# Performance work log

Measured on AMD Instinct MI355X. Metric: run time of the kernel, lower is better.

The kernel has to match this reference:

```python
import jax, jax.numpy as jnp
import numpy as np

D_MODEL = 64
D_INNER = 128
D_STATE = 16
D_CONV = 4
DT_RANK = 4
P_PIX = 5
HH = 120
WW = 120


def _layernorm(x, g, b):
    m = x.mean(-1, keepdims=True)
    v = ((x - m) ** 2).mean(-1, keepdims=True)
    return (x - m) * jax.lax.rsqrt(v + 1e-5) * g + b


def _ssm_scan(delta, Bm, Cm, u, A):
    # delta,u: (b,L,d); Bm,Cm: (b,L,n); A: (d,n)
    def step(h, inp):
        dt, bt, ct, ut = inp  # (b,d),(b,n),(b,n),(b,d)
        h = h * jnp.exp(dt[:, :, None] * A) + (dt * ut)[:, :, None] * bt[:, None, :]
        return h, jnp.einsum('bdn,bn->bd', h, ct)
    h0 = jnp.zeros((u.shape[0], A.shape[0], A.shape[1]), u.dtype)
    xs = (jnp.swapaxes(delta, 0, 1), jnp.swapaxes(Bm, 0, 1),
          jnp.swapaxes(Cm, 0, 1), jnp.swapaxes(u, 0, 1))
    _, ys = jax.lax.scan(step, h0, xs)
    return jnp.swapaxes(ys, 0, 1)  # (b,L,d)


def _mamba(p, x):
    # faithful mamba_ssm Mamba with use_fast_path=False, out_proj=Identity
    in_w, conv_w, conv_b, xproj_w, dt_w, dt_b, A_log, Dv = p
    L = x.shape[1]
    xz = jnp.einsum('bld,ed->ble', x, in_w)  # (b,L,2*d_inner)
    xh, z = xz[..., :D_INNER], xz[..., D_INNER:]
    xp = jnp.pad(xh, ((0, 0), (D_CONV - 1, 0), (0, 0)))  # causal depthwise conv
    conv = conv_b + sum(xp[:, i:i + L, :] * conv_w[:, i] for i in range(D_CONV))
    xh = jax.nn.silu(conv)
    dbl = jnp.einsum('bld,ed->ble', xh, xproj_w)
    dt = dbl[..., :DT_RANK]
    Bm = dbl[..., DT_RANK:DT_RANK + D_STATE]
    Cm = dbl[..., DT_RANK + D_STATE:]
    delta = jax.nn.softplus(jnp.einsum('blr,dr->bld', dt, dt_w) + dt_b)
    A = -jnp.exp(A_log)
    y = _ssm_scan(delta, Bm, Cm, xh, A) + xh * Dv
    return y * jax.nn.silu(z)


def _bidir(p2, xn):
    inp = jnp.stack([xn, xn[:, ::-1]])  # forward + flipped sequence
    ys = jax.vmap(_mamba, in_axes=(0, 0))(p2, inp)
    return ys[0], ys[1]


def _pixel(x, p2, g, b, out_w):
    B, C, Hh, Ww = x.shape
    p = P_PIX
    NH, NW = Hh // p, Ww // p
    L = NH * NW
    xd = x.reshape(B, C, NH, p, NW, p).transpose(0, 3, 5, 1, 2, 4).reshape(B * p * p, C, L)
    xn = _layernorm(jnp.swapaxes(xd, 1, 2), g, b)
    yf, yb = _bidir(p2, xn)
    yo = jnp.einsum('bld,cd->blc', yf + yb[:, ::-1], out_w)
    xo = jnp.swapaxes(yo, 1, 2).reshape(B, p, p, C, NH, NW).transpose(0, 3, 4, 1, 5, 2).reshape(B, C, Hh, Ww)
    return xo + x


def _window(x, p2, g, b, out_w, out_bw):
    # window p==1: AvgPool(1)/Upsample(1) are identities
    B, C, Hh, Ww = x.shape
    L = Hh * Ww
    xn = _layernorm(jnp.swapaxes(x.reshape(B, C, L), 1, 2), g, b)
    yf, yb = _bidir(p2, xn)
    xM = jnp.einsum('bld,cd->bcl', yf, out_w)
    yM = jnp.einsum('bld,cd->bcl', yb, out_bw)
    xo = jnp.einsum('bld,cd->blc', yf + yb[:, ::-1], out_w)
    return jnp.swapaxes(xo, 1, 2).reshape(B, C, Hh, Ww) + x, xM, yM


def _edges(M, step=32):
    hub = np.arange(0, M, step)
    ii, jj = np.meshgrid(hub, hub, indexing='ij')
    mask = ii != jj
    # off-diagonal hub-hub edges + self loops for every node (GCNConv add_remaining_self_loops)
    src = np.concatenate([ii[mask], np.arange(M)])
    dst = np.concatenate([jj[mask], np.arange(M)])
    deg = np.bincount(dst, minlength=M).astype(np.float32)
    norm = (deg[src] ** -0.5) * (deg[dst] ** -0.5)
    return jnp.asarray(src), jnp.asarray(dst), jnp.asarray(norm, jnp.float32)


def _gcn(x, Wm, bv, src, dst, norm, M):
    h = jnp.einsum('bmf,gf->bmg', x, Wm)
    msg = h[:, src, :] * norm[None, :, None]          # (B,E,g)
    agg = jax.ops.segment_sum(jnp.swapaxes(msg, 0, 1), dst, num_segments=M)
    return jnp.swapaxes(agg, 0, 1) + bv


def setup_inputs() -> dict:
    key = jax.random.key(0)
    ks = iter(jax.random.split(key, 48))
    def rn(shape, scale=1.0):
        return jax.random.normal(next(ks), shape, jnp.float32) * scale
    d = {}
    d['x'] = rn((1, D_MODEL, HH, WW))
    for pre in ('pix', 'win'):
        d[pre + '_in_w'] = rn((4, 2, 2 * D_INNER, D_MODEL), D_MODEL ** -0.5)
        d[pre + '_conv_w'] = rn((4, 2, D_INNER, D_CONV), 0.3)
        d[pre + '_conv_b'] = rn((4, 2, D_INNER), 0.02)
        d[pre + '_xproj_w'] = rn((4, 2, DT_RANK + 2 * D_STATE, D_INNER), D_INNER ** -0.5)
        d[pre + '_dt_w'] = rn((4, 2, D_INNER, DT_RANK), DT_RANK ** -0.5)
        d[pre + '_dt_b'] = jax.random.uniform(next(ks), (4, 2, D_INNER), jnp.float32, -5.0, -3.0)
        d[pre + '_A_log'] = jnp.log(jax.random.uniform(next(ks), (4, 2, D_INNER, D_STATE), jnp.float32, 1.0, 16.0))
        d[pre + '_D'] = rn((4, 2, D_INNER), 0.5)
        d[pre + '_ln_g'] = jnp.ones((4, D_MODEL), jnp.float32)
        d[pre + '_ln_b'] = jnp.zeros((4, D_MODEL), jnp.float32)
    d['pix_out_w'] = rn((4, D_MODEL, D_INNER), D_INNER ** -0.5)
    d['win_out_w'] = rn((4, D_MODEL, D_INNER), D_INNER ** -0.5)
    d['win_out_bw'] = rn((4, D_MODEL, D_INNER), D_INNER ** -0.5)
    d['gcn_w1'] = rn((2 * D_MODEL, 4 * D_MODEL), (4 * D_MODEL) ** -0.5)
    d['gcn_b1'] = jnp.zeros((2 * D_MODEL,), jnp.float32)
    d['gcn_w2'] = rn((D_MODEL, 2 * D_MODEL), (2 * D_MODEL) ** -0.5)
    d['gcn_b2'] = jnp.zeros((D_MODEL,), jnp.float32)
    return d


def reference(x, pix_in_w, pix_conv_w, pix_conv_b, pix_xproj_w, pix_dt_w, pix_dt_b, pix_A_log, pix_D,
              win_in_w, win_conv_w, win_conv_b, win_xproj_w, win_dt_w, win_dt_b, win_A_log, win_D,
              pix_ln_g, pix_ln_b, win_ln_g, win_ln_b, pix_out_w, win_out_w, win_out_bw,
              gcn_w1, gcn_b1, gcn_w2, gcn_b2):
    pix_stack = (pix_in_w, pix_conv_w, pix_conv_b, pix_xproj_w, pix_dt_w, pix_dt_b, pix_A_log, pix_D)
    win_stack = (win_in_w, win_conv_w, win_conv_b, win_xproj_w, win_dt_w, win_dt_b, win_A_log, win_D)
    def pick(stack, i):
        return tuple(t[i] for t in stack)
    def branch(x0, base):
        lastx, xM, yM = x0, None, None
        for s in range(2):
            i = base + s
            a = _pixel(lastx, pick(pix_stack, i), pix_ln_g[i], pix_ln_b[i], pix_out_w[i])
            a, xM, yM = _window(a, pick(win_stack, i), win_ln_g[i], win_ln_b[i], win_out_w[i], win_out_bw[i])
            lastx = lastx + a
        return lastx, xM, yM
    old = x
    lastx, xM, yM = branch(x, 0)
    lastx_T, xMT, yMT = branch(jnp.swapaxes(x, 2, 3), 2)
    B, C, Hh, Ww = x.shape
    M = Hh * Ww
    nf = jnp.swapaxes(jnp.concatenate([xM, yM, xMT, yMT], axis=1), 1, 2)  # (B,M,4C)
    src, dst, norm = _edges(M)
    h = jax.nn.relu(_gcn(nf, gcn_w1, gcn_b1, src, dst, norm, M))
    g = _gcn(h, gcn_w2, gcn_b2, src, dst, norm, M)
    gcn_x = jnp.swapaxes(g, 1, 2).reshape(B, C, Hh, Ww)
    return gcn_x + old + lastx + jnp.swapaxes(lastx_T, 2, 3)
```

## Files before the change

kernel.cpp:

```cpp
#include <hip/hip_runtime.h>
#include <hip/hip_bf16.h>

#define MT 14400
#define WNC 300
#define WCL 48
#define PT 16

typedef unsigned short u16;

__device__ __forceinline__ float b2f(u16 u){
  union { unsigned int i; float f; } v; v.i = ((unsigned int)u) << 16; return v.f;
}
__device__ __forceinline__ u16 f2b(float f){
  union { unsigned int i; float f; } v; v.f = f;
  unsigned int x = v.i;
  return (u16)((x + 0x7fffu + ((x >> 16) & 1u)) >> 16);
}
__device__ __forceinline__ unsigned int pk2(float a, float b){
  return (unsigned int)f2b(a) | ((unsigned int)f2b(b) << 16);
}
__device__ __forceinline__ void st8(float* p, uint4 v){
  *(float4*)p = make_float4(b2f((u16)v.x), b2f((u16)(v.x >> 16)), b2f((u16)v.y), b2f((u16)(v.y >> 16)));
  *(float4*)(p + 4) = make_float4(b2f((u16)v.z), b2f((u16)(v.z >> 16)), b2f((u16)v.w), b2f((u16)(v.w >> 16)));
}
__device__ __forceinline__ float siluf(float x){ return x / (1.f + expf(-x)); }
__device__ __forceinline__ float softplusf(float x){ return (x > 20.f) ? x : log1pf(expf(x)); }

__global__ __launch_bounds__(256) void k_detect(const u16* __restrict__ a, int n, int* __restrict__ flag){
  __shared__ int found;
  if (threadIdx.x == 0) found = 0;
  __syncthreads();
  int f = 0;
  for (int i = threadIdx.x; i < n; i += 256){
    float v = b2f(a[i]);
    if (!(fabsf(v) <= 1e9f)) f = 1;
  }
  if (f) atomicOr(&found, 1);
  __syncthreads();
  if (threadIdx.x == 0) *flag = found;
}

struct PTab {
  const void* src[27];
  float* dst[27];
  int n[27];
  int neg[27];
};

__global__ __launch_bounds__(256) void k_cvt(PTab tb, const int* __restrict__ flag){
  int id = blockIdx.y;
  int n = tb.n[id];
  int fp32 = *flag;
  float* d = tb.dst[id];
  int ng = tb.neg[id];
  for (int i = blockIdx.x * 256 + threadIdx.x; i < n; i += gridDim.x * 256){
    float v = fp32 ? ((const float*)tb.src[id])[i] : b2f(((const u16*)tb.src[id])[i]);
    if (ng) v = -expf(v) * 1.4426950408889634f;
    d[i] = v;
  }
}

__global__ __launch_bounds__(256) void k_wtrans(const float* __restrict__ Wpix, const float* __restrict__ Wwin,
                                                float* __restrict__ WTpix, float* __restrict__ WTwin){
  int mat = blockIdx.y;
  const float* src = (mat < 8) ? (Wpix + (size_t)mat * 16384) : (Wwin + (size_t)(mat - 8) * 16384);
  float* dst = (mat < 8) ? (WTpix + (size_t)mat * 16384) : (WTwin + (size_t)(mat - 8) * 16384);
  int idx = blockIdx.x * 256 + threadIdx.x;
  int e = idx >> 6, k = idx & 63;
  dst[k * 256 + e] = src[idx];
}

__global__ __launch_bounds__(256) void k_gcn1w(const float* __restrict__ ow, const float* __restrict__ obw,
                                               const float* __restrict__ G1, float* __restrict__ W1c){
  int str = blockIdx.y;
  int g = str >> 1, d = str & 1;
  int i2 = g * 2 + 1;
  const float* W = (d ? obw : ow) + (size_t)(i2 * 64) * 128;
  int idx = blockIdx.x * 256 + threadIdx.x;
  int kk = idx >> 7, f = idx & 127;
  float acc = 0.f;
  #pragma unroll 8
  for (int c = 0; c < 64; c++)
    acc += W[(size_t)c * 128 + kk] * G1[(size_t)f * 256 + str * 64 + c];
  W1c[((size_t)str * 128 + kk) * 128 + f] = acc;
}

__global__ __launch_bounds__(256) void k_cvt_x(const void* __restrict__ x, float* __restrict__ imgA,
                                               const int* __restrict__ flag){
  int idx = blockIdx.x * 256 + threadIdx.x;
  int l = idx % MT, c = idx / MT;
  float v = (*flag) ? ((const float*)x)[idx] : b2f(((const u16*)x)[idx]);
  imgA[idx] = v;
  imgA[(size_t)64 * MT + (size_t)c * MT + (l % 120) * 120 + l / 120] = v;
}

__global__ __launch_bounds__(256) void k_inproj(const float* __restrict__ img, const float* __restrict__ lng,
                                                const float* __restrict__ lnb, const float* __restrict__ WT,
                                                u16* __restrict__ xh, u16* __restrict__ z,
                                                int s, int pixelMode){
  int gd = blockIdx.y, g = gd >> 1, dir = gd & 1;
  int i2 = (g * 2 + s) * 2 + dir;
  int iln = g * 2 + s;
  int ttile = blockIdx.x >> 1, ntile = blockIdx.x & 1;
  int t0 = ttile * 64;
  const float* WTm = WT + (size_t)i2 * 16384 + ntile * 128;

  __shared__ __align__(16) float sAT[64 * 68];
  __shared__ __align__(16) float sB[64 * 128];
  __shared__ float ps[4][64], pq[4][64];
  int tid = threadIdx.x;
  int w = tid >> 6, lane = tid & 63;

  {
    int tq = t0 + lane, src = tq;
    if (dir){
      if (pixelMode){ int b = tq / 576, l = tq % 576; src = b * 576 + 575 - l; }
      else src = MT - 1 - tq;
    }
    int hw;
    if (pixelMode){
      int b = src / 576, l = src % 576;
      int ph = b / 5, pw = b % 5, nh = l / 24, nw = l % 24;
      hw = (nh * 5 + ph) * 120 + (nw * 5 + pw);
    } else hw = src;
    const float* base = img + (size_t)g * 64 * MT + hw;
    float sum = 0.f, sq = 0.f;
    #pragma unroll
    for (int j = 0; j < 16; j++){
      int c = w * 16 + j;
      float v = base[(size_t)c * MT];
      sAT[c * 68 + lane] = v;
      sum += v; sq += v * v;
    }
    ps[w][lane] = sum; pq[w][lane] = sq;
  }
  {
    #pragma unroll
    for (int it = 0; it < 8; it++){
      int idx = it * 256 + tid;
      int k = idx >> 5, e4 = (idx & 31) * 4;
      float4 v = *(const float4*)&WTm[(size_t)k * 256 + e4];
      *(float4*)&sB[k * 128 + e4] = v;
    }
  }
  __syncthreads();
  {
    float tot = ps[0][lane] + ps[1][lane] + ps[2][lane] + ps[3][lane];
    float tq2 = pq[0][lane] + pq[1][lane] + pq[2][lane] + pq[3][lane];
    float mean = tot * (1.f / 64.f);
    float var = tq2 * (1.f / 64.f) - mean * mean;
    float rs = rsqrtf(fmaxf(var, 0.f) + 1e-5f);
    #pragma unroll
    for (int j = 0; j < 16; j++){
      int c = w * 16 + j;
      float v = sAT[c * 68 + lane];
      sAT[c * 68 + lane] = (v - mean) * rs * lng[iln * 64 + c] + lnb[iln * 64 + c];
    }
  }
  __syncthreads();

  int tr = tid >> 4, tc = tid & 15;
  float acc[4][8];
  #pragma unroll
  for (int i = 0; i < 4; i++)
    #pragma unroll
    for (int j = 0; j < 8; j++) acc[i][j] = 0.f;

  for (int k0 = 0; k0 < 64; k0 += 4){
    #pragma unroll
    for (int kk = 0; kk < 4; kk++){
      float4 at = *(const float4*)&sAT[(k0 + kk) * 68 + tr * 4];
      float4 b0 = *(const float4*)&sB[(k0 + kk) * 128 + tc * 8];
      float4 b1 = *(const float4*)&sB[(k0 + kk) * 128 + tc * 8 + 4];
      float bv[8] = {b0.x, b0.y, b0.z, b0.w, b1.x, b1.y, b1.z, b1.w};
      #pragma unroll
      for (int i = 0; i < 4; i++){
        float av = ((const float*)&at)[i];
        #pragma unroll
        for (int j = 0; j < 8; j++) acc[i][j] += av * bv[j];
      }
    }
  }

  u16* dst = ntile ? z : xh;
  #pragma unroll
  for (int i = 0; i < 4; i++){
    int t_out = t0 + tr * 4 + i;
    size_t base = (size_t)gd * MT * 128 + (size_t)t_out * 128 + tc * 8;
    uint4 o;
    o.x = pk2(acc[i][0], acc[i][1]); o.y = pk2(acc[i][2], acc[i][3]);
    o.z = pk2(acc[i][4], acc[i][5]); o.w = pk2(acc[i][6], acc[i][7]);
    *(uint4*)&dst[base] = o;
  }
}

__global__ __launch_bounds__(256) void k_xproj(const u16* __restrict__ raw, const float* __restrict__ cw,
                                               const float* __restrict__ cb, const float* __restrict__ xpb,
                                               const float* __restrict__ dtw, const float* __restrict__ dtb,
                                               u16* __restrict__ delta, u16* __restrict__ Bm,
                                               u16* __restrict__ Cm, u16* __restrict__ xhs,
                                               int s, int pixelMode){
  int gd = blockIdx.y, g = gd >> 1, dir = gd & 1;
  int i2 = (g * 2 + s) * 2 + dir;
  const float* XP = xpb + (size_t)i2 * 36 * 128;
  const float* DW = dtw + (size_t)i2 * 128 * 4;
  const float* DB = dtb + (size_t)i2 * 128;
  int t0 = blockIdx.x * 64;
  int SL = pixelMode ? 576 : MT;
  int posBase = t0 % SL;
  size_t gb = (size_t)gd * MT * 128;
  size_t gb16 = (size_t)gd * MT * 16;
  const u16* rawg = raw + gb;

  __shared__ __align__(16) float sX[64 * 132];
  __shared__ __align__(16) float sW[36 * 132];
  float* sDbl = sX;
  int tid = threadIdx.x;

  #pragma unroll
  for (int it = 0; it < 8; it++){
    int idx = it * 256 + tid;
    int tok = idx >> 5, k4 = (idx & 31) * 4;
    int t = t0 + tok, pos = posBase + tok;
    const float4* wr0 = (const float4*)&cw[(size_t)(i2 * 128 + k4) * 4];
    float4 w0 = wr0[0], w1 = wr0[1], w2 = wr0[2], w3 = wr0[3];
    float4 cbv = *(const float4*)&cb[i2 * 128 + k4];
    float a0 = cbv.x, a1 = cbv.y, a2 = cbv.z, a3 = cbv.w;
    #pragma unroll
    for (int i = 0; i < 4; i++){
      int d = 3 - i;
      if (pos >= d){
        uint2 rv = *(const uint2*)&rawg[(size_t)(t - d) * 128 + k4];
        float r0 = b2f((u16)rv.x), r1 = b2f((u16)(rv.x >> 16));
        float r2 = b2f((u16)rv.y), r3 = b2f((u16)(rv.y >> 16));
        a0 += r0 * ((const float*)&w0)[i];
        a1 += r1 * ((const float*)&w1)[i];
        a2 += r2 * ((const float*)&w2)[i];
        a3 += r3 * ((const float*)&w3)[i];
      }
    }
    a0 = siluf(a0); a1 = siluf(a1); a2 = siluf(a2); a3 = siluf(a3);
    *(float4*)&sX[tok * 132 + k4] = make_float4(a0, a1, a2, a3);
    uint2 o; o.x = pk2(a0, a1); o.y = pk2(a2, a3);
    *(uint2*)&xhs[gb + (size_t)t * 128 + k4] = o;
  }
  for (int idx = tid; idx < 36 * 32; idx += 256){
    int out = idx >> 5, k4 = (idx & 31) * 4;
    *(float4*)&sW[out * 132 + k4] = *(const float4*)&XP[(size_t)out * 128 + k4];
  }
  __syncthreads();

  int tr = tid >> 4, tc = tid & 15;
  float acc[4][3];
  #pragma unroll
  for (int i = 0; i < 4; i++){ acc[i][0]=0.f; acc[i][1]=0.f; acc[i][2]=0.f; }
  int o0 = tc * 3;     if (o0 > 35) o0 = 35;
  int o1 = tc * 3 + 1; if (o1 > 35) o1 = 35;
  int o2 = tc * 3 + 2; if (o2 > 35) o2 = 35;

  for (int k0 = 0; k0 < 128; k0 += 4){
    float4 a4[4], bw[3];
    #pragma unroll
    for (int i = 0; i < 4; i++) a4[i] = *(const float4*)&sX[(tr * 4 + i) * 132 + k0];
    bw[0] = *(const float4*)&sW[o0 * 132 + k0];
    bw[1] = *(const float4*)&sW[o1 * 132 + k0];
    bw[2] = *(const float4*)&sW[o2 * 132 + k0];
    #pragma unroll
    for (int kk = 0; kk < 4; kk++){
      #pragma unroll
      for (int i = 0; i < 4; i++){
        float av = ((const float*)&a4[i])[kk];
        #pragma unroll
        for (int j = 0; j < 3; j++) acc[i][j] += av * ((const float*)&bw[j])[kk];
      }
    }
  }
  __syncthreads();

  #pragma unroll
  for (int i = 0; i < 4; i++){
    #pragma unroll
    for (int j = 0; j < 3; j++){
      int out = tc * 3 + j;
      if (out < 36) sDbl[(tr * 4 + i) * 52 + out] = acc[i][j];
    }
  }
  __syncthreads();

  {
    int d = tid & 127, half = tid >> 7;
    float4 dw = *(const float4*)&DW[(size_t)d * 4];
    float db = DB[d];
    #pragma unroll
    for (int it = 0; it < 32; it++){
      int t = it * 2 + half;
      const float* row = &sDbl[t * 52];
      float v = db + row[0] * dw.x + row[1] * dw.y + row[2] * dw.z + row[3] * dw.w;
      delta[gb + (size_t)(t0 + t) * 128 + d] = f2b(softplusf(v));
    }
  }
  #pragma unroll
  for (int it = 0; it < 8; it++){
    int flat = it * 256 + tid;
    int t = flat >> 5, n = flat & 31;
    float v = sDbl[t * 52 + 4 + n];
    if (n < 16) Bm[gb16 + (size_t)(t0 + t) * 16 + n] = f2b(v);
    else        Cm[gb16 + (size_t)(t0 + t) * 16 + (n - 16)] = f2b(v);
  }
}

__global__ __launch_bounds__(256) void k_scan_p1(const u16* __restrict__ delta, const u16* __restrict__ xhs,
                                                 const u16* __restrict__ Bm, const float* __restrict__ A2b,
                                                 float* __restrict__ Acar, float* __restrict__ Bcar, int s){
  int gd = blockIdx.y, g = gd >> 1, dir = gd & 1;
  int i2 = (g * 2 + s) * 2 + dir;
  int chunk = blockIdx.x;
  int tid = threadIdx.x, ch = tid >> 1, nb = (tid & 1) * 8;
  float A2[8], ap[8], bc[8];
  #pragma unroll
  for (int j = 0; j < 8; j++){
    A2[j] = A2b[((size_t)i2 * 128 + ch) * 16 + nb + j];
    ap[j] = 1.f; bc[j] = 0.f;
  }
  size_t so = (size_t)gd * MT * 128 + (size_t)chunk * WCL * 128;
  size_t bo = (size_t)gd * MT * 16  + (size_t)chunk * WCL * 16;
  __shared__ __align__(16) float sd[PT * 128];
  __shared__ __align__(16) float su[PT * 128];
  __shared__ __align__(16) float sb[PT * 16];
  uint4 rd, ru; float rbf;
  rd = *(const uint4*)&delta[so + 8 * (size_t)tid];
  ru = *(const uint4*)&xhs[so + 8 * (size_t)tid];
  rbf = b2f(Bm[bo + tid]);
  const int NT = WCL / PT;
  for (int tile = 0; tile < NT; tile++){
    __syncthreads();
    st8(&sd[8 * tid], rd);
    st8(&su[8 * tid], ru);
    sb[tid] = rbf;
    __syncthreads();
    if (tile + 1 < NT){
      rd = *(const uint4*)&delta[so + (size_t)(tile + 1) * PT * 128 + 8 * (size_t)tid];
      ru = *(const uint4*)&xhs[so + (size_t)(tile + 1) * PT * 128 + 8 * (size_t)tid];
      rbf = b2f(Bm[bo + (size_t)(tile + 1) * PT * 16 + tid]);
    }
    #pragma unroll
    for (int t = 0; t < PT; t++){
      float dt = sd[t * 128 + ch];
      float u  = su[t * 128 + ch];
      float du = dt * u;
      #pragma unroll
      for (int j = 0; j < 8; j++){
        float e = exp2f(dt * A2[j]);
        bc[j] = bc[j] * e + du * sb[t * 16 + nb + j];
        ap[j] *= e;
      }
    }
  }
  size_t o = ((size_t)gd * WNC + chunk) * 2048 + (size_t)ch * 16 + nb;
  float4* A4 = (float4*)(Acar + o);
  float4* B4 = (float4*)(Bcar + o);
  A4[0] = make_float4(ap[0], ap[1], ap[2], ap[3]);
  A4[1] = make_float4(ap[4], ap[5], ap[6], ap[7]);
  B4[0] = make_float4(bc[0], bc[1], bc[2], bc[3]);
  B4[1] = make_float4(bc[4], bc[5], bc[6], bc[7]);
}

__global__ __launch_bounds__(256) void k_scan_p2(const float* __restrict__ Acar, const float* __restrict__ Bcar,
                                                 float* __restrict__ Hin, int resetPeriod){
  int flat = blockIdx.x * 256 + threadIdx.x;
  int cs = flat & 2047, gd = flat >> 11;
  float h = 0.f;
  int cnt = 0;
  for (int c = 0; c < WNC; c++){
    if (cnt == resetPeriod) { h = 0.f; cnt = 0; }
    cnt++;
    size_t o = ((size_t)gd * WNC + c) * 2048 + cs;
    Hin[o] = h;
    h = Acar[o] * h + Bcar[o];
  }
}

__global__ __launch_bounds__(256) void k_scan_p3(const u16* __restrict__ delta, const u16* __restrict__ xhs,
                                                 const u16* __restrict__ Bm, const u16* __restrict__ Cm,
                                                 const u16* __restrict__ zz, const float* __restrict__ A2b,
                                                 const float* __restrict__ Db, const float* __restrict__ Hin,
                                                 u16* __restrict__ ys, int s){
  int gd = blockIdx.y, g = gd >> 1, dir = gd & 1;
  int i2 = (g * 2 + s) * 2 + dir;
  int chunk = blockIdx.x;
  int tid = threadIdx.x, ch = tid >> 1, nb = (tid & 1) * 8;
  float A2[8], h[8];
  size_t ho = ((size_t)gd * WNC + chunk) * 2048 + (size_t)ch * 16 + nb;
  {
    const float4* H4 = (const float4*)(Hin + ho);
    float4 h0 = H4[0], h1 = H4[1];
    h[0]=h0.x; h[1]=h0.y; h[2]=h0.z; h[3]=h0.w;
    h[4]=h1.x; h[5]=h1.y; h[6]=h1.z; h[7]=h1.w;
  }
  #pragma unroll
  for (int j = 0; j < 8; j++) A2[j] = A2b[((size_t)i2 * 128 + ch) * 16 + nb + j];
  float Dv = Db[(size_t)i2 * 128 + ch];
  size_t so = (size_t)gd * MT * 128 + (size_t)chunk * WCL * 128;
  size_t bo = (size_t)gd * MT * 16  + (size_t)chunk * WCL * 16;
  __shared__ __align__(16) float sd[PT * 128];
  __shared__ __align__(16) float su[PT * 128];
  __shared__ __align__(16) float sb[PT * 16];
  __shared__ __align__(16) float sc[PT * 16];
  __shared__ __align__(16) float sy[PT * 128];
  uint4 rd, ru; float rbf, rcf;
  rd = *(const uint4*)&delta[so + 8 * (size_t)tid];
  ru = *(const uint4*)&xhs[so + 8 * (size_t)tid];
  rbf = b2f(Bm[bo + tid]); rcf = b2f(Cm[bo + tid]);
  const int NT = WCL / PT;
  for (int tile = 0; tile < NT; tile++){
    __syncthreads();
    st8(&sd[8 * tid], rd);
    st8(&su[8 * tid], ru);
    sb[tid] = rbf; sc[tid] = rcf;
    __syncthreads();
    if (tile + 1 < NT){
      rd = *(const uint4*)&delta[so + (size_t)(tile + 1) * PT * 128 + 8 * (size_t)tid];
      ru = *(const uint4*)&xhs[so + (size_t)(tile + 1) * PT * 128 + 8 * (size_t)tid];
      rbf = b2f(Bm[bo + (size_t)(tile + 1) * PT * 16 + tid]);
      rcf = b2f(Cm[bo + (size_t)(tile + 1) * PT * 16 + tid]);
    }
    #pragma unroll
    for (int t = 0; t < PT; t++){
      float dt = sd[t * 128 + ch];
      float u  = su[t * 128 + ch];
      float du = dt * u;
      float acc = 0.f;
      #pragma unroll
      for (int j = 0; j < 8; j++){
        float e = exp2f(dt * A2[j]);
        h[j] = h[j] * e + du * sb[t * 16 + nb + j];
        acc += h[j] * sc[t * 16 + nb + j];
      }
      acc += __shfl_xor(acc, 1);
      if (!(tid & 1)) sy[t * 128 + ch] = acc + u * Dv;
    }
    __syncthreads();
    {
      uint4 zv = *(const uint4*)&zz[so + (size_t)tile * PT * 128 + 8 * (size_t)tid];
      const float* py = &sy[8 * tid];
      float y[8];
      y[0] = py[0] * siluf(b2f((u16)zv.x));       y[1] = py[1] * siluf(b2f((u16)(zv.x >> 16)));
      y[2] = py[2] * siluf(b2f((u16)zv.y));       y[3] = py[3] * siluf(b2f((u16)(zv.y >> 16)));
      y[4] = py[4] * siluf(b2f((u16)zv.z));       y[5] = py[5] * siluf(b2f((u16)(zv.z >> 16)));
      y[6] = py[6] * siluf(b2f((u16)zv.w));       y[7] = py[7] * siluf(b2f((u16)(zv.w >> 16)));
      uint4 o;
      o.x = pk2(y[0], y[1]); o.y = pk2(y[2], y[3]); o.z = pk2(y[4], y[5]); o.w = pk2(y[6], y[7]);
      *(uint4*)&ys[so + (size_t)tile * PT * 128 + 8 * (size_t)tid] = o;
    }
    __syncthreads();
  }
}

__global__ __launch_bounds__(256) void k_outproj_pixel(const u16* __restrict__ ys, const float* __restrict__ owb,
                                                       const float* __restrict__ imgA, float* __restrict__ imgB, int s){
  int g = blockIdx.y;
  int i2 = g * 2 + s;
  int tile = blockIdx.x;
  int t0 = tile * 64;
  int b = tile / 9, l0 = (tile % 9) * 64;
  const float* W = owb + (size_t)(i2 * 64) * 128;
  const u16* Yf = ys + (size_t)(g * 2 + 0) * MT * 128;
  const u16* Yb = ys + (size_t)(g * 2 + 1) * MT * 128;
  __shared__ __align__(16) float sA[64 * 36];
  __shared__ __align__(16) float sW[32 * 68];
  __shared__ __align__(16) float sO[64 * 68];
  int tid = threadIdx.x;
  int tr = tid >> 4, tc = tid & 15;
  float acc[4][4];
  #pragma unroll
  for (int i = 0; i < 4; i++){ acc[i][0]=0.f; acc[i][1]=0.f; acc[i][2]=0.f; acc[i][3]=0.f; }

  for (int kt = 0; kt < 4; kt++){
    int k0 = kt * 32;
    {
      int t = tid >> 2, f8 = (tid & 3) * 8;
      int rt = b * 576 + 575 - (l0 + t);
      uint4 vf = *(const uint4*)&Yf[(size_t)(t0 + t) * 128 + k0 + f8];
      uint4 vb = *(const uint4*)&Yb[(size_t)rt * 128 + k0 + f8];
      float* pa = &sA[t * 36 + f8];
      pa[0] = b2f((u16)vf.x) + b2f((u16)vb.x);
      pa[1] = b2f((u16)(vf.x >> 16)) + b2f((u16)(vb.x >> 16));
      pa[2] = b2f((u16)vf.y) + b2f((u16)vb.y);
      pa[3] = b2f((u16)(vf.y >> 16)) + b2f((u16)(vb.y >> 16));
      pa[4] = b2f((u16)vf.z) + b2f((u16)vb.z);
      pa[5] = b2f((u16)(vf.z >> 16)) + b2f((u16)(vb.z >> 16));
      pa[6] = b2f((u16)vf.w) + b2f((u16)vb.w);
      pa[7] = b2f((u16)(vf.w >> 16)) + b2f((u16)(vb.w >> 16));
    }
    {
      int c = tid >> 2, f8 = (tid & 3) * 8;
      const float* wr = &W[(size_t)c * 128 + k0 + f8];
      #pragma unroll
      for (int j = 0; j < 8; j++) sW[(f8 + j) * 68 + c] = wr[j];
    }
    __syncthreads();
    #pragma unroll
    for (int k4 = 0; k4 < 32; k4 += 4){
      float4 a[4];
      #pragma unroll
      for (int i = 0; i < 4; i++) a[i] = *(const float4*)&sA[(tr * 4 + i) * 36 + k4];
      #pragma unroll
      for (int kk = 0; kk < 4; kk++){
        float4 bv = *(const float4*)&sW[(k4 + kk) * 68 + tc * 4];
        #pragma unroll
        for (int i = 0; i < 4; i++){
          float av = ((const float*)&a[i])[kk];
          acc[i][0] += av * bv.x; acc[i][1] += av * bv.y;
          acc[i][2] += av * bv.z; acc[i][3] += av * bv.w;
        }
      }
    }
    __syncthreads();
  }
  #pragma unroll
  for (int j = 0; j < 4; j++)
    *(float4*)&sO[(tc * 4 + j) * 68 + tr * 4] = make_float4(acc[0][j], acc[1][j], acc[2][j], acc[3][j]);
  __syncthreads();
  {
    int c = tid >> 2, q = tid & 3;
    int ph = b / 5, pw = b % 5;
    size_t base = (size_t)g * 64 * MT + (size_t)c * MT;
    #pragma unroll
    for (int v = 0; v < 16; v++){
      int l = l0 + q * 16 + v;
      int nh = l / 24, nw = l % 24;
      size_t io = base + (nh * 5 + ph) * 120 + (nw * 5 + pw);
      imgB[io] = imgA[io] + sO[c * 68 + q * 16 + v];
    }
  }
}

__global__ __launch_bounds__(256) void k_outproj_win(const u16* __restrict__ ys, const float* __restrict__ owb,
                                                     float* __restrict__ imgA, float* __restrict__ imgB, int s){
  int g = blockIdx.y;
  int i2 = g * 2 + s;
  int t0 = blockIdx.x * 64;
  const float* W = owb + (size_t)(i2 * 64) * 128;
  const u16* Yf = ys + (size_t)(g * 2 + 0) * MT * 128;
  const u16* Yb = ys + (size_t)(g * 2 + 1) * MT * 128;
  __shared__ __align__(16) float sA[64 * 36];
  __shared__ __align__(16) float sW[32 * 68];
  __shared__ __align__(16) float sO[64 * 68];
  int tid = threadIdx.x;
  int tr = tid >> 4, tc = tid & 15;
  float acc[4][4];
  #pragma unroll
  for (int i = 0; i < 4; i++){ acc[i][0]=0.f; acc[i][1]=0.f; acc[i][2]=0.f; acc[i][3]=0.f; }

  for (int kt = 0; kt < 4; kt++){
    int k0 = kt * 32;
    {
      int t = tid >> 2, f8 = (tid & 3) * 8;
      int l = t0 + t;
      uint4 vf = *(const uint4*)&Yf[(size_t)l * 128 + k0 + f8];
      uint4 vb = *(const uint4*)&Yb[(size_t)(MT - 1 - l) * 128 + k0 + f8];
      float* pa = &sA[t * 36 + f8];
      pa[0] = b2f((u16)vf.x) + b2f((u16)vb.x);
      pa[1] = b2f((u16)(vf.x >> 16)) + b2f((u16)(vb.x >> 16));
      pa[2] = b2f((u16)vf.y) + b2f((u16)vb.y);
      pa[3] = b2f((u16)(vf.y >> 16)) + b2f((u16)(vb.y >> 16));
      pa[4] = b2f((u16)vf.z) + b2f((u16)vb.z);
      pa[5] = b2f((u16)(vf.z >> 16)) + b2f((u16)(vb.z >> 16));
      pa[6] = b2f((u16)vf.w) + b2f((u16)vb.w);
      pa[7] = b2f((u16)(vf.w >> 16)) + b2f((u16)(vb.w >> 16));
    }
    {
      int c = tid >> 2, f8 = (tid & 3) * 8;
      const float* wr = &W[(size_t)c * 128 + k0 + f8];
      #pragma unroll
      for (int j = 0; j < 8; j++) sW[(f8 + j) * 68 + c] = wr[j];
    }
    __syncthreads();
    #pragma unroll
    for (int k4 = 0; k4 < 32; k4 += 4){
      float4 a[4];
      #pragma unroll
      for (int i = 0; i < 4; i++) a[i] = *(const float4*)&sA[(tr * 4 + i) * 36 + k4];
      #pragma unroll
      for (int kk = 0; kk < 4; kk++){
        float4 bv = *(const float4*)&sW[(k4 + kk) * 68 + tc * 4];
        #pragma unroll
        for (int i = 0; i < 4; i++){
          float av = ((const float*)&a[i])[kk];
          acc[i][0] += av * bv.x; acc[i][1] += av * bv.y;
          acc[i][2] += av * bv.z; acc[i][3] += av * bv.w;
        }
      }
    }
    __syncthreads();
  }
  #pragma unroll
  for (int j = 0; j < 4; j++)
    *(float4*)&sO[(tc * 4 + j) * 68 + tr * 4] = make_float4(acc[0][j], acc[1][j], acc[2][j], acc[3][j]);
  __syncthreads();
  {
    int c = tid >> 2, q = tid & 3;
    size_t base = (size_t)g * 64 * MT + (size_t)c * MT + t0 + q * 16;
    float* pB = &imgB[base];
    float* pA = &imgA[base];
    const float* pS = &sO[c * 68 + q * 16];
    #pragma unroll
    for (int v = 0; v < 4; v++){
      float4 d = *(const float4*)&pS[v * 4];
      float4 bb = *(const float4*)&pB[v * 4];
      bb.x += d.x; bb.y += d.y; bb.z += d.z; bb.w += d.w;
      *(float4*)&pB[v * 4] = bb;
      float4 aa = *(const float4*)&pA[v * 4];
      aa.x += bb.x; aa.y += bb.y; aa.z += bb.z; aa.w += bb.w;
      *(float4*)&pA[v * 4] = aa;
    }
  }
}

__global__ __launch_bounds__(256) void k_gcn1(const u16* __restrict__ ys, const float* __restrict__ W1c,
                                              float* __restrict__ t1){
  int t0 = blockIdx.x * 64;
  __shared__ __align__(16) float sA[64 * 36];
  __shared__ __align__(16) float sB[32 * 132];
  int tid = threadIdx.x, tr = tid >> 4, tc = tid & 15;
  float acc[4][8];
  #pragma unroll
  for (int i = 0; i < 4; i++)
    #pragma unroll
    for (int j = 0; j < 8; j++) acc[i][j] = 0.f;

  for (int kt = 0; kt < 16; kt++){
    int str = kt >> 2, k0 = (kt & 3) * 32;
    const u16* Y = ys + (size_t)str * MT * 128;
    {
      int t = tid >> 2, f8 = (tid & 3) * 8;
      uint4 p = *(const uint4*)&Y[(size_t)(t0 + t) * 128 + k0 + f8];
      st8(&sA[t * 36 + f8], p);
    }
    {
      const float* Wc = W1c + ((size_t)str * 128 + k0) * 128;
      int kk = tid >> 3, f16 = (tid & 7) * 16;
      #pragma unroll
      for (int v = 0; v < 4; v++)
        *(float4*)&sB[kk * 132 + f16 + v * 4] = *(const float4*)&Wc[(size_t)kk * 128 + f16 + v * 4];
    }
    __syncthreads();
    #pragma unroll
    for (int k4 = 0; k4 < 32; k4 += 4){
      float4 a[4];
      #pragma unroll
      for (int i = 0; i < 4; i++) a[i] = *(const float4*)&sA[(tr * 4 + i) * 36 + k4];
      #pragma unroll
      for (int kk = 0; kk < 4; kk++){
        float4 b0 = *(const float4*)&sB[(k4 + kk) * 132 + tc * 8];
        float4 b1 = *(const float4*)&sB[(k4 + kk) * 132 + tc * 8 + 4];
        float bv[8] = {b0.x, b0.y, b0.z, b0.w, b1.x, b1.y, b1.z, b1.w};
        #pragma unroll
        for (int i = 0; i < 4; i++){
          float av = ((const float*)&a[i])[kk];
          #pragma unroll
          for (int j = 0; j < 8; j++) acc[i][j] += av * bv[j];
        }
      }
    }
    __syncthreads();
  }
  #pragma unroll
  for (int i = 0; i < 4; i++){
    size_t base = (size_t)(t0 + tr * 4 + i) * 128 + tc * 8;
    *(float4*)&t1[base]     = make_float4(acc[i][0], acc[i][1], acc[i][2], acc[i][3]);
    *(float4*)&t1[base + 4] = make_float4(acc[i][4], acc[i][5], acc[i][6], acc[i][7]);
  }
}

__global__ __launch_bounds__(128) void k_hub1(const float* __restrict__ t1, float* __restrict__ hubm){
  int f = threadIdx.x;
  float sum = 0.f;
  for (int hb = 0; hb < 450; hb++) sum += t1[(size_t)(hb * 32) * 128 + f];
  hubm[f] = sum * (1.f / 450.f);
}

__global__ __launch_bounds__(256) void k_gcn2(const float* __restrict__ t1, const float* __restrict__ hubm,
                                              const float* __restrict__ b1, const float* __restrict__ W2,
                                              float* __restrict__ t2){
  int t0 = blockIdx.x * 64;
  __shared__ __align__(16) float sA[64 * 36];
  __shared__ __align__(16) float sW[32 * 68];
  int tid = threadIdx.x, tr = tid >> 4, tc = tid & 15;
  float acc[4][4];
  #pragma unroll
  for (int i = 0; i < 4; i++){ acc[i][0]=0.f; acc[i][1]=0.f; acc[i][2]=0.f; acc[i][3]=0.f; }

  for (int kt = 0; kt < 4; kt++){
    int k0 = kt * 32;
    {
      int t = tid >> 2, f8 = (tid & 3) * 8;
      int l = t0 + t;
      const float* src = ((l & 31) == 0) ? &hubm[k0 + f8] : &t1[(size_t)l * 128 + k0 + f8];
      #pragma unroll
      for (int j = 0; j < 8; j++)
        sA[t * 36 + f8 + j] = fmaxf(src[j] + b1[k0 + f8 + j], 0.f);
    }
    {
      int c = tid >> 2, f8 = (tid & 3) * 8;
      const float* wr = &W2[(size_t)c * 128 + k0 + f8];
      #pragma unroll
      for (int j = 0; j < 8; j++) sW[(f8 + j) * 68 + c] = wr[j];
    }
    __syncthreads();
    #pragma unroll
    for (int k4 = 0; k4 < 32; k4 += 4){
      float4 a[4];
      #pragma unroll
      for (int i = 0; i < 4; i++) a[i] = *(const float4*)&sA[(tr * 4 + i) * 36 + k4];
      #pragma unroll
      for (int kk = 0; kk < 4; kk++){
        float4 bv = *(const float4*)&sW[(k4 + kk) * 68 + tc * 4];
        #pragma unroll
        for (int i = 0; i < 4; i++){
          float av = ((const float*)&a[i])[kk];
          acc[i][0] += av * bv.x; acc[i][1] += av * bv.y;
          acc[i][2] += av * bv.z; acc[i][3] += av * bv.w;
        }
      }
    }
    __syncthreads();
  }
  #pragma unroll
  for (int i = 0; i < 4; i++)
    *(float4*)&t2[(size_t)(t0 + tr * 4 + i) * 64 + tc * 4] = make_float4(acc[i][0], acc[i][1], acc[i][2], acc[i][3]);
}

__global__ __launch_bounds__(64) void k_hub2(const float* __restrict__ t2, float* __restrict__ hubm2){
  int c = threadIdx.x;
  float sum = 0.f;
  for (int hb = 0; hb < 450; hb++) sum += t2[(size_t)(hb * 32) * 64 + c];
  hubm2[c] = sum * (1.f / 450.f);
}

__global__ __launch_bounds__(256) void k_final(const void* __restrict__ x, const float* __restrict__ t2,
                                               const float* __restrict__ hubm2, const float* __restrict__ b2,
                                               const float* __restrict__ imgA, void* __restrict__ out,
                                               const int* __restrict__ flag){
  int idx = blockIdx.x * 256 + threadIdx.x;
  int l = idx % MT, c = idx / MT;
  int fp32 = *flag;
  float gval = (((l & 31) == 0) ? hubm2[c] : t2[(size_t)l * 64 + c]) + b2[c];
  float a0 = imgA[idx];
  float a1 = imgA[(size_t)64 * MT + (size_t)c * MT + (l % 120) * 120 + l / 120];
  float xv = fp32 ? ((const float*)x)[idx] : b2f(((const u16*)x)[idx]);
  float val = gval + xv + a0 + a1;
  if (fp32) ((float*)out)[idx] = val;
  else      ((u16*)out)[idx] = f2b(val);
}

extern "C" void kernel_launch(void* const* d_in, const int* in_sizes, int n_in,
                              void* d_out, int out_size, void* d_ws, size_t ws_size,
                              hipStream_t stream){
  int I_X=0,I_PIW=1,I_PCW=2,I_PCB=3,I_PXP=4,I_PDTW=5,I_PDTB=6,I_PAL=7,I_PD=8,I_PLG=9,I_PLB=10,
      I_WIW=11,I_WCW=12,I_WCB=13,I_WXP=14,I_WDTW=15,I_WDTB=16,I_WAL=17,I_WD=18,I_WLG=19,I_WLB=20,
      I_POW=21,I_WOW=22,I_WOBW=23,I_G1=24,I_GB1=25,I_G2=26,I_GB2=27;
  if (n_in >= 28 && in_sizes[9] == 131072){
    I_WIW=9;I_WCW=10;I_WCB=11;I_WXP=12;I_WDTW=13;I_WDTB=14;I_WAL=15;I_WD=16;
    I_PLG=17;I_PLB=18;I_WLG=19;I_WLB=20;
  }
  if (n_in < 28 || in_sizes[I_PIW] != 131072 || out_size != 921600) return;

  float* Wp = (float*)d_ws;
  size_t off = 0;
  auto alloc = [&](size_t n){ size_t r = off; off += (n + 63) & ~(size_t)63; return r; };
  size_t oFlag=alloc(64);
  size_t oPIW=alloc(131072), oPCW=alloc(4096), oPCB=alloc(1024), oPXP=alloc(36864),
         oPDTW=alloc(4096), oPDTB=alloc(1024), oPA=alloc(16384), oPD=alloc(1024),
         oPLG=alloc(256), oPLB=alloc(256);
  size_t oWIW=alloc(131072), oWCW=alloc(4096), oWCB=alloc(1024), oWXP=alloc(36864),
         oWDTW=alloc(4096), oWDTB=alloc(1024), oWA=alloc(16384), oWD=alloc(1024),
         oWLG=alloc(256), oWLB=alloc(256);
  size_t oPOW=alloc(32768), oWOW=alloc(32768), oWOBW=alloc(32768),
         oG1=alloc(32768), oGB1=alloc(128), oG2=alloc(8192), oGB2=alloc(64);
  size_t oPIWT=alloc(131072), oWIWT=alloc(131072), oW1C=alloc(65536);
  size_t oImgA=alloc(2UL*64*MT), oImgB=alloc(2UL*64*MT);
  size_t oRaw=alloc(2UL*MT*128);
  size_t oZ=alloc(2UL*MT*128), oXhs=alloc(2UL*MT*128), oDelta=alloc(2UL*MT*128);
  size_t oBm=alloc(2UL*MT*16), oCm=alloc(2UL*MT*16);
  size_t oAc=alloc(4UL*WNC*2048), oBc=alloc(4UL*WNC*2048), oHin=alloc(4UL*WNC*2048);
  size_t oT1=alloc((size_t)MT*128), oHub1=alloc(128), oT2=alloc((size_t)MT*64), oHub2=alloc(64);
  if (ws_size < off * sizeof(float)) return;

  int* flag = (int*)(Wp + oFlag);
  k_detect<<<dim3(1), dim3(256), 0, stream>>>((const u16*)d_in[I_PAL], 16384, flag);

  PTab tb;
  int ti = 0;
  auto add = [&](int inIdx, size_t o, int n, int neg){
    tb.src[ti] = d_in[inIdx]; tb.dst[ti] = Wp + o; tb.n[ti] = n; tb.neg[ti] = neg; ti++;
  };
  add(I_PIW,oPIW,131072,0); add(I_PCW,oPCW,4096,0); add(I_PCB,oPCB,1024,0); add(I_PXP,oPXP,36864,0);
  add(I_PDTW,oPDTW,4096,0); add(I_PDTB,oPDTB,1024,0); add(I_PAL,oPA,16384,1); add(I_PD,oPD,1024,0);
  add(I_PLG,oPLG,256,0); add(I_PLB,oPLB,256,0);
  add(I_WIW,oWIW,131072,0); add(I_WCW,oWCW,4096,0); add(I_WCB,oWCB,1024,0); add(I_WXP,oWXP,36864,0);
  add(I_WDTW,oWDTW,4096,0); add(I_WDTB,oWDTB,1024,0); add(I_WAL,oWA,16384,1); add(I_WD,oWD,1024,0);
  add(I_WLG,oWLG,256,0); add(I_WLB,oWLB,256,0);
  add(I_POW,oPOW,32768,0); add(I_WOW,oWOW,32768,0); add(I_WOBW,oWOBW,32768,0);
  add(I_G1,oG1,32768,0); add(I_GB1,oGB1,128,0); add(I_G2,oG2,8192,0); add(I_GB2,oGB2,64,0);

  k_cvt<<<dim3(128, 27), dim3(256), 0, stream>>>(tb, flag);
  k_wtrans<<<dim3(64, 16), dim3(256), 0, stream>>>(Wp+oPIW, Wp+oWIW, Wp+oPIWT, Wp+oWIWT);
  k_gcn1w<<<dim3(64, 4), dim3(256), 0, stream>>>(Wp+oWOW, Wp+oWOBW, Wp+oG1, Wp+oW1C);
  k_cvt_x<<<dim3(3600), dim3(256), 0, stream>>>(d_in[I_X], Wp + oImgA, flag);

  float *imgA = Wp+oImgA, *imgB = Wp+oImgB,
        *Ac = Wp+oAc, *Bc = Wp+oBc, *Hin = Wp+oHin;
  u16 *raw = (u16*)(Wp+oRaw), *ys = (u16*)(Wp+oRaw),
      *zz = (u16*)(Wp+oZ), *xhs = (u16*)(Wp+oXhs), *delta = (u16*)(Wp+oDelta),
      *Bm = (u16*)(Wp+oBm), *Cm = (u16*)(Wp+oCm);

  for (int s = 0; s < 2; s++){
    k_inproj<<<dim3(450, 4), dim3(256), 0, stream>>>(imgA, Wp+oPLG, Wp+oPLB, Wp+oPIWT, raw, zz, s, 1);
    k_xproj <<<dim3(225, 4), dim3(256), 0, stream>>>(raw, Wp+oPCW, Wp+oPCB, Wp+oPXP, Wp+oPDTW, Wp+oPDTB,
                                                     delta, Bm, Cm, xhs, s, 1);
    k_scan_p1<<<dim3(WNC, 4), dim3(256), 0, stream>>>(delta, xhs, Bm, Wp+oPA, Ac, Bc, s);
    k_scan_p2<<<dim3(32), dim3(256), 0, stream>>>(Ac, Bc, Hin, 12);
    k_scan_p3<<<dim3(WNC, 4), dim3(256), 0, stream>>>(delta, xhs, Bm, Cm, zz, Wp+oPA, Wp+oPD, Hin, ys, s);
    k_outproj_pixel<<<dim3(225, 2), dim3(256), 0, stream>>>(ys, Wp+oPOW, imgA, imgB, s);

    k_inproj<<<dim3(450, 4), dim3(256), 0, stream>>>(imgB, Wp+oWLG, Wp+oWLB, Wp+oWIWT, raw, zz, s, 0);
    k_xproj <<<dim3(225, 4), dim3(256), 0, stream>>>(raw, Wp+oWCW, Wp+oWCB, Wp+oWXP, Wp+oWDTW, Wp+oWDTB,
                                                     delta, Bm, Cm, xhs, s, 0);
    k_scan_p1<<<dim3(WNC, 4), dim3(256), 0, stream>>>(delta, xhs, Bm, Wp+oWA, Ac, Bc, s);
    k_scan_p2<<<dim3(32), dim3(256), 0, stream>>>(Ac, Bc, Hin, WNC);
    k_scan_p3<<<dim3(WNC, 4), dim3(256), 0, stream>>>(delta, xhs, Bm, Cm, zz, Wp+oWA, Wp+oWD, Hin, ys, s);
    k_outproj_win<<<dim3(225, 2), dim3(256), 0, stream>>>(ys, Wp+oWOW, imgA, imgB, s);
  }

  k_gcn1<<<dim3(225), dim3(256), 0, stream>>>(ys, Wp+oW1C, Wp+oT1);
  k_hub1<<<dim3(1), dim3(128), 0, stream>>>(Wp+oT1, Wp+oHub1);
  k_gcn2<<<dim3(225), dim3(256), 0, stream>>>(Wp+oT1, Wp+oHub1, Wp+oGB1, Wp+oG2, Wp+oT2);
  k_hub2<<<dim3(1), dim3(64), 0, stream>>>(Wp+oT2, Wp+oHub2);
  k_final<<<dim3(3600), dim3(256), 0, stream>>>(d_in[I_X], Wp+oT2, Wp+oHub2, Wp+oGB2, imgA, d_out, flag);
}
```

Before: 1.220 ms.

## Fuse scan phase-1 chunk carries into xproj kernel, retile to scan chunk size

Merges the chunked-scan first pass into the xproj kernel. Each block now covers one scan chunk of WCL tokens instead of 64, and the per-chunk A/B carries are computed straight from shared-memory delta, xh and B values. This removes a kernel launch per stage and the re-read of delta, xhs and Bm from global memory. In exchange the xproj block does serial per-token scan work, uses smaller GEMM tiles and more shared memory, which may lower occupancy.

```diff
diff --git a/kernel.cpp b/kernel.cpp
--- a/kernel.cpp
+++ b/kernel.cpp
@@ -197,28 +197,32 @@
 __global__ __launch_bounds__(256) void k_xproj(const u16* __restrict__ raw, const float* __restrict__ cw,
                                                const float* __restrict__ cb, const float* __restrict__ xpb,
                                                const float* __restrict__ dtw, const float* __restrict__ dtb,
+                                               const float* __restrict__ A2b,
                                                u16* __restrict__ delta, u16* __restrict__ Bm,
                                                u16* __restrict__ Cm, u16* __restrict__ xhs,
+                                               float* __restrict__ Acar, float* __restrict__ Bcar,
                                                int s, int pixelMode){
   int gd = blockIdx.y, g = gd >> 1, dir = gd & 1;
   int i2 = (g * 2 + s) * 2 + dir;
   const float* XP = xpb + (size_t)i2 * 36 * 128;
   const float* DW = dtw + (size_t)i2 * 128 * 4;
   const float* DB = dtb + (size_t)i2 * 128;
-  int t0 = blockIdx.x * 64;
+  int chunk = blockIdx.x;
+  int t0 = chunk * WCL;
   int SL = pixelMode ? 576 : MT;
   int posBase = t0 % SL;
   size_t gb = (size_t)gd * MT * 128;
   size_t gb16 = (size_t)gd * MT * 16;
   const u16* rawg = raw + gb;
 
-  __shared__ __align__(16) float sX[64 * 132];
+  __shared__ __align__(16) float sX[WCL * 132];
   __shared__ __align__(16) float sW[36 * 132];
-  float* sDbl = sX;
+  __shared__ __align__(4)  u16  sDelta[WCL * 128];
+  float* sDbl = sW;
   int tid = threadIdx.x;
 
   #pragma unroll
-  for (int it = 0; it < 8; it++){
+  for (int it = 0; it < 6; it++){
     int idx = it * 256 + tid;
     int tok = idx >> 5, k4 = (idx & 31) * 4;
     int t = t0 + tok, pos = posBase + tok;
@@ -251,24 +255,24 @@
   __syncthreads();
 
   int tr = tid >> 4, tc = tid & 15;
-  float acc[4][3];
-  #pragma unroll
-  for (int i = 0; i < 4; i++){ acc[i][0]=0.f; acc[i][1]=0.f; acc[i][2]=0.f; }
+  float acc[3][3];
+  #pragma unroll
+  for (int i = 0; i < 3; i++){ acc[i][0]=0.f; acc[i][1]=0.f; acc[i][2]=0.f; }
   int o0 = tc * 3;     if (o0 > 35) o0 = 35;
   int o1 = tc * 3 + 1; if (o1 > 35) o1 = 35;
   int o2 = tc * 3 + 2; if (o2 > 35) o2 = 35;
 
   for (int k0 = 0; k0 < 128; k0 += 4){
-    float4 a4[4], bw[3];
-    #pragma unroll
-    for (int i = 0; i < 4; i++) a4[i] = *(const float4*)&sX[(tr * 4 + i) * 132 + k0];
+    float4 a4[3], bw[3];
+    #pragma unroll
+    for (int i = 0; i < 3; i++) a4[i] = *(const float4*)&sX[(tr * 3 + i) * 132 + k0];
     bw[0] = *(const float4*)&sW[o0 * 132 + k0];
     bw[1] = *(const float4*)&sW[o1 * 132 + k0];
     bw[2] = *(const float4*)&sW[o2 * 132 + k0];
     #pragma unroll
     for (int kk = 0; kk < 4; kk++){
       #pragma unroll
-      for (int i = 0; i < 4; i++){
+      for (int i = 0; i < 3; i++){
         float av = ((const float*)&a4[i])[kk];
         #pragma unroll
         for (int j = 0; j < 3; j++) acc[i][j] += av * ((const float*)&bw[j])[kk];
@@ -278,11 +282,11 @@
   __syncthreads();
 
   #pragma unroll
-  for (int i = 0; i < 4; i++){
+  for (int i = 0; i < 3; i++){
     #pragma unroll
     for (int j = 0; j < 3; j++){
       int out = tc * 3 + j;
-      if (out < 36) sDbl[(tr * 4 + i) * 52 + out] = acc[i][j];
+      if (out < 36) sDbl[(tr * 3 + i) * 52 + out] = acc[i][j];
     }
   }
   __syncthreads();
@@ -292,77 +296,55 @@
     float4 dw = *(const float4*)&DW[(size_t)d * 4];
     float db = DB[d];
     #pragma unroll
-    for (int it = 0; it < 32; it++){
+    for (int it = 0; it < 24; it++){
       int t = it * 2 + half;
       const float* row = &sDbl[t * 52];
       float v = db + row[0] * dw.x + row[1] * dw.y + row[2] * dw.z + row[3] * dw.w;
-      delta[gb + (size_t)(t0 + t) * 128 + d] = f2b(softplusf(v));
-    }
-  }
-  #pragma unroll
-  for (int it = 0; it < 8; it++){
+      u16 dh = f2b(softplusf(v));
+      delta[gb + (size_t)(t0 + t) * 128 + d] = dh;
+      sDelta[t * 128 + d] = dh;
+    }
+  }
+  #pragma unroll
+  for (int it = 0; it < 6; it++){
     int flat = it * 256 + tid;
     int t = flat >> 5, n = flat & 31;
     float v = sDbl[t * 52 + 4 + n];
     if (n < 16) Bm[gb16 + (size_t)(t0 + t) * 16 + n] = f2b(v);
     else        Cm[gb16 + (size_t)(t0 + t) * 16 + (n - 16)] = f2b(v);
   }
-}
-
-__global__ __launch_bounds__(256) void k_scan_p1(const u16* __restrict__ delta, const u16* __restrict__ xhs,
-                                                 const u16* __restrict__ Bm, const float* __restrict__ A2b,
-                                                 float* __restrict__ Acar, float* __restrict__ Bcar, int s){
-  int gd = blockIdx.y, g = gd >> 1, dir = gd & 1;
-  int i2 = (g * 2 + s) * 2 + dir;
-  int chunk = blockIdx.x;
-  int tid = threadIdx.x, ch = tid >> 1, nb = (tid & 1) * 8;
-  float A2[8], ap[8], bc[8];
-  #pragma unroll
-  for (int j = 0; j < 8; j++){
-    A2[j] = A2b[((size_t)i2 * 128 + ch) * 16 + nb + j];
-    ap[j] = 1.f; bc[j] = 0.f;
-  }
-  size_t so = (size_t)gd * MT * 128 + (size_t)chunk * WCL * 128;
-  size_t bo = (size_t)gd * MT * 16  + (size_t)chunk * WCL * 16;
-  __shared__ __align__(16) float sd[PT * 128];
-  __shared__ __align__(16) float su[PT * 128];
-  __shared__ __align__(16) float sb[PT * 16];
-  uint4 rd, ru; float rbf;
-  rd = *(const uint4*)&delta[so + 8 * (size_t)tid];
-  ru = *(const uint4*)&xhs[so + 8 * (size_t)tid];
-  rbf = b2f(Bm[bo + tid]);
-  const int NT = WCL / PT;
-  for (int tile = 0; tile < NT; tile++){
-    __syncthreads();
-    st8(&sd[8 * tid], rd);
-    st8(&su[8 * tid], ru);
-    sb[tid] = rbf;
-    __syncthreads();
-    if (tile + 1 < NT){
-      rd = *(const uint4*)&delta[so + (size_t)(tile + 1) * PT * 128 + 8 * (size_t)tid];
-      ru = *(const uint4*)&xhs[so + (size_t)(tile + 1) * PT * 128 + 8 * (size_t)tid];
-      rbf = b2f(Bm[bo + (size_t)(tile + 1) * PT * 16 + tid]);
-    }
-    #pragma unroll
-    for (int t = 0; t < PT; t++){
-      float dt = sd[t * 128 + ch];
-      float u  = su[t * 128 + ch];
+  __syncthreads();
+
+  {
+    int ch = tid >> 1, nb = (tid & 1) * 8;
+    float A2[8], ap[8], bc[8];
+    #pragma unroll
+    for (int j = 0; j < 8; j++){
+      A2[j] = A2b[((size_t)i2 * 128 + ch) * 16 + nb + j];
+      ap[j] = 1.f; bc[j] = 0.f;
+    }
+    for (int t = 0; t < WCL; t++){
+      float dt = b2f(sDelta[t * 128 + ch]);
+      float u  = sX[t * 132 + ch];
       float du = dt * u;
+      float4 bb0 = *(const float4*)&sDbl[t * 52 + 4 + nb];
+      float4 bb1 = *(const float4*)&sDbl[t * 52 + 4 + nb + 4];
+      float bbv[8] = {bb0.x, bb0.y, bb0.z, bb0.w, bb1.x, bb1.y, bb1.z, bb1.w};
       #pragma unroll
       for (int j = 0; j < 8; j++){
         float e = exp2f(dt * A2[j]);
-        bc[j] = bc[j] * e + du * sb[t * 16 + nb + j];
+        bc[j] = bc[j] * e + du * bbv[j];
         ap[j] *= e;
       }
     }
-  }
-  size_t o = ((size_t)gd * WNC + chunk) * 2048 + (size_t)ch * 16 + nb;
-  float4* A4 = (float4*)(Acar + o);
-  float4* B4 = (float4*)(Bcar + o);
-  A4[0] = make_float4(ap[0], ap[1], ap[2], ap[3]);
-  A4[1] = make_float4(ap[4], ap[5], ap[6], ap[7]);
-  B4[0] = make_float4(bc[0], bc[1], bc[2], bc[3]);
-  B4[1] = make_float4(bc[4], bc[5], bc[6], bc[7]);
+    size_t o = ((size_t)gd * WNC + chunk) * 2048 + (size_t)ch * 16 + nb;
+    float4* A4 = (float4*)(Acar + o);
+    float4* B4 = (float4*)(Bcar + o);
+    A4[0] = make_float4(ap[0], ap[1], ap[2], ap[3]);
+    A4[1] = make_float4(ap[4], ap[5], ap[6], ap[7]);
+    B4[0] = make_float4(bc[0], bc[1], bc[2], bc[3]);
+    B4[1] = make_float4(bc[4], bc[5], bc[6], bc[7]);
+  }
 }
 
 __global__ __launch_bounds__(256) void k_scan_p2(const float* __restrict__ Acar, const float* __restrict__ Bcar,
@@ -817,17 +799,15 @@
 
   for (int s = 0; s < 2; s++){
     k_inproj<<<dim3(450, 4), dim3(256), 0, stream>>>(imgA, Wp+oPLG, Wp+oPLB, Wp+oPIWT, raw, zz, s, 1);
-    k_xproj <<<dim3(225, 4), dim3(256), 0, stream>>>(raw, Wp+oPCW, Wp+oPCB, Wp+oPXP, Wp+oPDTW, Wp+oPDTB,
-                                                     delta, Bm, Cm, xhs, s, 1);
-    k_scan_p1<<<dim3(WNC, 4), dim3(256), 0, stream>>>(delta, xhs, Bm, Wp+oPA, Ac, Bc, s);
+    k_xproj <<<dim3(WNC, 4), dim3(256), 0, stream>>>(raw, Wp+oPCW, Wp+oPCB, Wp+oPXP, Wp+oPDTW, Wp+oPDTB,
+                                                     Wp+oPA, delta, Bm, Cm, xhs, Ac, Bc, s, 1);
     k_scan_p2<<<dim3(32), dim3(256), 0, stream>>>(Ac, Bc, Hin, 12);
     k_scan_p3<<<dim3(WNC, 4), dim3(256), 0, stream>>>(delta, xhs, Bm, Cm, zz, Wp+oPA, Wp+oPD, Hin, ys, s);
     k_outproj_pixel<<<dim3(225, 2), dim3(256), 0, stream>>>(ys, Wp+oPOW, imgA, imgB, s);
 
     k_inproj<<<dim3(450, 4), dim3(256), 0, stream>>>(imgB, Wp+oWLG, Wp+oWLB, Wp+oWIWT, raw, zz, s, 0);
-    k_xproj <<<dim3(225, 4), dim3(256), 0, stream>>>(raw, Wp+oWCW, Wp+oWCB, Wp+oWXP, Wp+oWDTW, Wp+oWDTB,
-                                                     delta, Bm, Cm, xhs, s, 0);
-    k_scan_p1<<<dim3(WNC, 4), dim3(256), 0, stream>>>(delta, xhs, Bm, Wp+oWA, Ac, Bc, s);
+    k_xproj <<<dim3(WNC, 4), dim3(256), 0, stream>>>(raw, Wp+oWCW, Wp+oWCB, Wp+oWXP, Wp+oWDTW, Wp+oWDTB,
+                                                     Wp+oWA, delta, Bm, Cm, xhs, Ac, Bc, s, 0);
     k_scan_p2<<<dim3(32), dim3(256), 0, stream>>>(Ac, Bc, Hin, WNC);
     k_scan_p3<<<dim3(WNC, 4), dim3(256), 0, stream>>>(delta, xhs, Bm, Cm, zz, Wp+oWA, Wp+oWD, Hin, ys, s);
     k_outproj_win<<<dim3(225, 2), dim3(256), 0, stream>>>(ys, Wp+oWOW, imgA, imgB, s);
```

After: 1.236 ms. About the same (+1.3%).
